# Optimization experiments

Measured on AMD Instinct MI355X. Metric: run time of the kernel, lower is better.

## Reference

```python
import jax, jax.numpy as jnp
import numpy as np

B, K = 512, 64
EBD, VFD = 256, 512
SENS = EBD + VFD            # 768 sensory inputs to layer 0
LAYERS = [512, 256, 64]     # inter, command, motor neurons (NCP wiring)


def _make_layer_params(key, in_features, hidden):
    ks = jax.random.split(key, 9)
    cat = in_features + hidden
    s = 1.0 / np.sqrt(cat)
    def lin(k):
        return jax.random.normal(k, (hidden, cat), dtype=jnp.float32) * s
    # sparsity mask: random NCP-style sparsity on the input block, dense recurrent block
    in_mask = (jax.random.uniform(ks[8], (hidden, in_features)) < 0.5).astype(jnp.float32)
    rec_mask = jnp.ones((hidden, hidden), dtype=jnp.float32)
    mask = jnp.concatenate([in_mask, rec_mask], axis=1)  # (hidden, in+hidden)
    return dict(
        ff1_w=lin(ks[0]), ff1_b=jnp.zeros((hidden,), jnp.float32),
        ff2_w=lin(ks[1]), ff2_b=jnp.zeros((hidden,), jnp.float32),
        ta_w=lin(ks[2]), ta_b=jnp.zeros((hidden,), jnp.float32),
        tb_w=lin(ks[3]), tb_b=jnp.zeros((hidden,), jnp.float32),
        mask=mask,
    )


def setup_inputs() -> dict:
    key = jax.random.key(0)
    k_base, k_vis, k0, k1, k2 = jax.random.split(key, 5)
    inp = {
        'base_expanded_seq': jax.random.normal(k_base, (B, K, EBD), dtype=jnp.float32),
        'visual_seq': jax.random.normal(k_vis, (B, K, VFD), dtype=jnp.float32),
    }
    in_feats = [SENS, LAYERS[0], LAYERS[1]]
    for li, (k, fin, hid) in enumerate(zip([k0, k1, k2], in_feats, LAYERS)):
        p = _make_layer_params(k, fin, hid)
        for name, v in p.items():
            inp[f'l{li}_{name}'] = v
    return inp


def _cfc_cell(x_in, h, ff1_w, ff1_b, ff2_w, ff2_b, ta_w, ta_b, tb_w, tb_b, mask, ts=1.0):
    # ncps CfCCell, mode='default', no backbone, sparsity mask on ff1/ff2
    x = jnp.concatenate([x_in, h], axis=-1)          # (B, in+hidden)
    ff1 = jnp.tanh(x @ (ff1_w * mask).T + ff1_b)
    ff2 = jnp.tanh(x @ (ff2_w * mask).T + ff2_b)
    t_a = x @ ta_w.T + ta_b
    t_b = x @ tb_w.T + tb_b
    t_interp = jax.nn.sigmoid(t_a * ts + t_b)
    return ff1 * (1.0 - t_interp) + t_interp * ff2


def reference(base_expanded_seq, visual_seq,
              l0_ff1_w, l0_ff1_b, l0_ff2_w, l0_ff2_b, l0_ta_w, l0_ta_b, l0_tb_w, l0_tb_b, l0_mask,
              l1_ff1_w, l1_ff1_b, l1_ff2_w, l1_ff2_b, l1_ta_w, l1_ta_b, l1_tb_w, l1_tb_b, l1_mask,
              l2_ff1_w, l2_ff1_b, l2_ff2_w, l2_ff2_b, l2_ta_w, l2_ta_b, l2_tb_w, l2_tb_b, l2_mask):
    layers = [
        (l0_ff1_w, l0_ff1_b, l0_ff2_w, l0_ff2_b, l0_ta_w, l0_ta_b, l0_tb_w, l0_tb_b, l0_mask),
        (l1_ff1_w, l1_ff1_b, l1_ff2_w, l1_ff2_b, l1_ta_w, l1_ta_b, l1_tb_w, l1_tb_b, l1_mask),
        (l2_ff1_w, l2_ff1_b, l2_ff2_w, l2_ff2_b, l2_ta_w, l2_ta_b, l2_tb_w, l2_tb_b, l2_mask),
    ]
    b = base_expanded_seq.shape[0]
    x_seq = jnp.concatenate([base_expanded_seq, visual_seq], axis=-1)  # (B,K,768)
    x_seq = jnp.swapaxes(x_seq, 0, 1)                                  # (K,B,768)
    h_init = tuple(jnp.zeros((b, h), dtype=x_seq.dtype) for h in LAYERS)

    def step(carry, x_t):
        inp = x_t
        new_hs = []
        for p, h in zip(layers, carry):
            h_new = _cfc_cell(inp, h, *p)
            inp = h_new
            new_hs.append(h_new)
        return tuple(new_hs), None

    final_h, _ = jax.lax.scan(step, h_init, x_seq)
    return final_h[-1]  # (B, motor_neurons) = last timestep motor-layer output
```

## Files before the change

### kernel.cpp

```cpp
#include <hip/hip_runtime.h>
#include <cmath>


typedef __attribute__((ext_vector_type(8))) _Float16 half8;
typedef __attribute__((ext_vector_type(4))) float f32x4;

#define DEVINL __device__ __forceinline__

struct Params {
  const float* base;
  const float* visual;
  const _Float16 *w0, *w1, *w2;
  const float *b0f1,*b0f2,*b0ta,*b0tb;
  const float *b1f1,*b1f2,*b1ta,*b1tb;
  const float *b2f1,*b2f2,*b2ta,*b2tb;
  _Float16 *xh0,*xl0,*xh1,*xl1;
  _Float16 *h0h0,*h0h1,*h0l0,*h0l1;
  _Float16 *h1h0,*h1h1,*h1l0,*h1l1;
  _Float16 *h2h0,*h2h1,*h2l0,*h2l1;
  float* out;
};

DEVINL void gload(half8& d, const _Float16* a) {
  asm volatile("global_load_dwordx4 %0, %1, off" : "=v"(d) : "v"(a));
}
template <int V>
DEVINL void vmwait() {
  __builtin_amdgcn_s_waitcnt((V & 15) | (7 << 4) | (15 << 8) | ((V >> 4) << 14));
  __builtin_amdgcn_sched_barrier(0);
}

template <int C, int NC, int D, class AF>
DEVINL void pipe_iter(half8 (&buf)[D][6], f32x4 (&acc)[4], const AF& addr) {
  constexpr int issued = (C + D < NC) ? (C + D) : NC;
  vmwait<6 * (issued - C - 1)>();
  {
    half8 b0 = buf[C % D][0], b1 = buf[C % D][1];
    half8 b2 = buf[C % D][2], b3 = buf[C % D][3];
    half8 ah = buf[C % D][4], al = buf[C % D][5];
    acc[0] = __builtin_amdgcn_mfma_f32_16x16x32_f16(ah, b0, acc[0], 0, 0, 0);
    acc[0] = __builtin_amdgcn_mfma_f32_16x16x32_f16(al, b0, acc[0], 0, 0, 0);
    acc[1] = __builtin_amdgcn_mfma_f32_16x16x32_f16(ah, b1, acc[1], 0, 0, 0);
    acc[1] = __builtin_amdgcn_mfma_f32_16x16x32_f16(al, b1, acc[1], 0, 0, 0);
    acc[2] = __builtin_amdgcn_mfma_f32_16x16x32_f16(ah, b2, acc[2], 0, 0, 0);
    acc[2] = __builtin_amdgcn_mfma_f32_16x16x32_f16(al, b2, acc[2], 0, 0, 0);
    acc[3] = __builtin_amdgcn_mfma_f32_16x16x32_f16(ah, b3, acc[3], 0, 0, 0);
    acc[3] = __builtin_amdgcn_mfma_f32_16x16x32_f16(al, b3, acc[3], 0, 0, 0);
  }
  if constexpr (C + D < NC) {
#pragma unroll
    for (int j = 0; j < 6; ++j) gload(buf[C % D][j], addr(C + D, j));
  }
  if constexpr (C + 1 < NC) pipe_iter<C + 1, NC, D>(buf, acc, addr);
}

template <int NC, class AF>
DEVINL void gemm_pipe(f32x4 (&acc)[4], const AF& addr) {
  constexpr int D = (NC < 4) ? NC : 4;
  half8 buf[D][6];
#pragma unroll
  for (int c = 0; c < D; ++c)
#pragma unroll
    for (int j = 0; j < 6; ++j) gload(buf[c][j], addr(c, j));
  pipe_iter<0, NC, D>(buf, acc, addr);
}

DEVINL void run_xprep(const Params& p, int t, int b ) {
  _Float16* xh = (t & 1) ? p.xh1 : p.xh0;
  _Float16* xl = (t & 1) ? p.xl1 : p.xl0;
  int tid = b * 256 + threadIdx.x;
#pragma unroll
  for (int i = tid; i < 49152; i += 12288) {
    int m = i / 96;
    int k = (i - m * 96) * 8;
    const float* src = (k < 256) ? (p.base + (m * 64 + t) * 256 + k)
                                 : (p.visual + (m * 64 + t) * 512 + (k - 256));
    const f32x4* q = (const f32x4*)src;
    f32x4 v0 = q[0], v1 = q[1];
    half8 hh, ll;
#pragma unroll
    for (int j = 0; j < 4; ++j) {
      _Float16 a = (_Float16)v0[j]; hh[j] = a;     ll[j]     = (_Float16)(v0[j] - (float)a);
      _Float16 c = (_Float16)v1[j]; hh[j + 4] = c; ll[j + 4] = (_Float16)(v1[j] - (float)c);
    }
    int off = (((m >> 4) * 24 + (k >> 5)) * 64 + ((k >> 3) & 3) * 16 + (m & 15)) * 8;
    *(half8*)(xh + off) = hh;
    *(half8*)(xl + off) = ll;
  }
}

template <int L>
DEVINL void run_rec(const Params& p, int t, int b) {
  constexpr int HH = (L == 0) ? 512 : ((L == 1) ? 256 : 64);
  constexpr int NC = (L == 0) ? 40 : ((L == 1) ? 24 : 10);
  constexpr int NCH = HH / 32;

  const int lane = threadIdx.x & 63, wv = threadIdx.x >> 6;
  const int lr = lane & 15, lq = lane >> 4;
  int mt, nt;
  if constexpr (L == 0)      { mt = b >> 5; nt = b & 31; }
  else if constexpr (L == 1) { mt = b >> 4; nt = b & 15; }
  else                       { mt = b >> 2; nt = b & 3; }
  const int m_base = mt * 64 + wv * 16, n0 = nt * 16;
  const int mt16 = mt * 4 + wv;
  const int wbuf = t & 1;

  const _Float16 *hph, *hpl, *pah = nullptr, *pal = nullptr;
  _Float16 *oh, *ol;
  const float *bf1p, *bf2p, *btap, *btbp;
  const _Float16* wpk;
  if constexpr (L == 0) {
    wpk = p.w0 + (nt * 40) * 512 + lane * 8;
    pah = wbuf ? p.xh1 : p.xh0;    pal = wbuf ? p.xl1 : p.xl0;
    hph = wbuf ? p.h0h0 : p.h0h1;  hpl = wbuf ? p.h0l0 : p.h0l1;
    oh  = wbuf ? p.h0h1 : p.h0h0;  ol  = wbuf ? p.h0l1 : p.h0l0;
    bf1p = p.b0f1; bf2p = p.b0f2; btap = p.b0ta; btbp = p.b0tb;
  } else if constexpr (L == 1) {
    wpk = p.w1 + (nt * 24) * 512 + lane * 8;
    pah = wbuf ? p.h0h1 : p.h0h0;  pal = wbuf ? p.h0l1 : p.h0l0;
    hph = wbuf ? p.h1h0 : p.h1h1;  hpl = wbuf ? p.h1l0 : p.h1l1;
    oh  = wbuf ? p.h1h1 : p.h1h0;  ol  = wbuf ? p.h1l1 : p.h1l0;
    bf1p = p.b1f1; bf2p = p.b1f2; btap = p.b1ta; btbp = p.b1tb;
  } else {
    wpk = p.w2 + (nt * 10) * 512 + lane * 8;
    pah = wbuf ? p.h1h1 : p.h1h0;  pal = wbuf ? p.h1l1 : p.h1l0;
    hph = wbuf ? p.h2h0 : p.h2h1;  hpl = wbuf ? p.h2l0 : p.h2l1;
    oh  = wbuf ? p.h2h1 : p.h2h0;  ol  = wbuf ? p.h2l1 : p.h2l0;
    bf1p = p.b2f1; bf2p = p.b2f2; btap = p.b2ta; btbp = p.b2tb;
  }

  f32x4 acc[4];
#pragma unroll
  for (int g = 0; g < 4; ++g) acc[g] = f32x4{0.f, 0.f, 0.f, 0.f};

  const int lane8 = lane * 8;
  auto addr = [&](int c, int j) -> const _Float16* {
    if constexpr (L == 0) {
      if (j < 4) return wpk + (j * (32 * 40) + c) * 512;
      if (c < 24) return ((j == 4) ? pah : pal) + (mt16 * 24 + c) * 512 + lane8;
      return ((j == 4) ? hph : hpl) + (mt16 * 16 + (c - 24)) * 512 + lane8;
    } else if constexpr (L == 1) {
      if (j < 4) return wpk + (j * (16 * 24) + c) * 512;
      if (c < 16) return ((j == 4) ? pah : pal) + (mt16 * 16 + c) * 512 + lane8;
      return ((j == 4) ? hph : hpl) + (mt16 * 8 + (c - 16)) * 512 + lane8;
    } else {
      if (j < 4) return wpk + (j * (4 * 10) + c) * 512;
      if (c < 8) return ((j == 4) ? pah : pal) + (mt16 * 8 + c) * 512 + lane8;
      return ((j == 4) ? hph : hpl) + (mt16 * 2 + (c - 8)) * 512 + lane8;
    }
  };
  gemm_pipe<NC>(acc, addr);

  const int n = n0 + lr;
  const float bff1 = bf1p[n], bff2 = bf2p[n], bta = btap[n], btb = btbp[n];
  const int obase = ((m_base >> 4) * NCH + (n >> 5)) * 512 + ((n >> 3) & 3) * 128 + (n & 7);
#pragma unroll
  for (int r = 0; r < 4; ++r) {
    const int row = m_base + lq * 4 + r;
    const int lrr = lq * 4 + r;
    float a0 = acc[0][r], a1 = acc[1][r], a2 = acc[2][r], a3 = acc[3][r];
    float vf1 = a0 + bff1;
    float vf2 = a1 + bff2;
    float vt  = (a2 + bta) + (a3 + btb);
    float ff1 = tanhf(vf1);
    float ff2 = tanhf(vf2);
    float ti  = 1.0f / (1.0f + __expf(-vt));
    float hv  = ff1 + ti * (ff2 - ff1);
    _Float16 hh = (_Float16)hv;
    oh[obase + lrr * 8] = hh;
    ol[obase + lrr * 8] = (_Float16)(hv - (float)hh);
    if constexpr (L == 2) {
      if (t == 63) p.out[row * 64 + n] = hv;
    }
  }
}

__global__ __launch_bounds__(256, 2) void cfc_step(Params p, int s) {
  const int bid = blockIdx.x;
  if (bid < 48)       { int t = s + 1; if (t >= 0 && t < 64) run_xprep(p, t, bid); }
  else if (bid < 304) { int t = s;     if (t >= 0 && t < 64) run_rec<0>(p, t, bid - 48); }
  else if (bid < 432) { int t = s - 1; if (t >= 0 && t < 64) run_rec<1>(p, t, bid - 304); }
  else                { int t = s - 2; if (t >= 0 && t < 64) run_rec<2>(p, t, bid - 432); }
}

__global__ void prep_w_pk(const float* __restrict__ w, const float* __restrict__ mask,
                          _Float16* __restrict__ dst, int WK, int total) {
  int i = blockIdx.x * 256 + threadIdx.x;
  if (i >= total) return;
  int e = i & 7, lane = (i >> 3) & 63, rem = i >> 9;
  int NCk = WK >> 5;
  int c = rem % NCk, nt = rem / NCk;
  int n = nt * 16 + (lane & 15);
  int k = c * 32 + (lane >> 4) * 8 + e;
  float v = w[n * WK + k];
  if (mask) v *= mask[n * WK + k];
  dst[i] = (_Float16)v;
}

__global__ void zero_kernel(unsigned* __restrict__ p, int n) {
  int i = blockIdx.x * 256 + threadIdx.x;
  if (i < n) p[i] = 0u;
}

extern "C" void kernel_launch(void* const* d_in, const int* in_sizes, int n_in,
                              void* d_out, int out_size, void* d_ws, size_t ws_size,
                              hipStream_t stream) {
  _Float16* w0  = (_Float16*)d_ws;
  _Float16* w1  = w0 + 2621440;
  _Float16* w2  = w1 + 786432;
  _Float16* xh0 = w2 + 81920;
  _Float16* xl0 = xh0 + 393216;
  _Float16* xh1 = xl0 + 393216;
  _Float16* xl1 = xh1 + 393216;
  _Float16* hb  = xl1 + 393216;
  _Float16* h0h0 = hb;            _Float16* h0h1 = h0h0 + 262144;
  _Float16* h0l0 = h0h1 + 262144; _Float16* h0l1 = h0l0 + 262144;
  _Float16* h1h0 = h0l1 + 262144; _Float16* h1h1 = h1h0 + 131072;
  _Float16* h1l0 = h1h1 + 131072; _Float16* h1l1 = h1l0 + 131072;
  _Float16* h2h0 = h1l1 + 131072; _Float16* h2h1 = h2h0 + 32768;
  _Float16* h2l0 = h2h1 + 32768;  _Float16* h2l1 = h2l0 + 32768;

  const int h_uints = 1703936 / 2;
  zero_kernel<<<(h_uints + 255) / 256, 256, 0, stream>>>((unsigned*)hb, h_uints);

  const float* F = nullptr;
  auto in = [&](int i) { return (const float*)d_in[i]; };

  prep_w_pk<<<2560, 256, 0, stream>>>(in(2),  in(10), w0 + 0 * 655360, 1280, 655360);
  prep_w_pk<<<2560, 256, 0, stream>>>(in(4),  in(10), w0 + 1 * 655360, 1280, 655360);
  prep_w_pk<<<2560, 256, 0, stream>>>(in(6),  F,      w0 + 2 * 655360, 1280, 655360);
  prep_w_pk<<<2560, 256, 0, stream>>>(in(8),  F,      w0 + 3 * 655360, 1280, 655360);
  prep_w_pk<<<768,  256, 0, stream>>>(in(11), in(19), w1 + 0 * 196608, 768,  196608);
  prep_w_pk<<<768,  256, 0, stream>>>(in(13), in(19), w1 + 1 * 196608, 768,  196608);
  prep_w_pk<<<768,  256, 0, stream>>>(in(15), F,      w1 + 2 * 196608, 768,  196608);
  prep_w_pk<<<768,  256, 0, stream>>>(in(17), F,      w1 + 3 * 196608, 768,  196608);
  prep_w_pk<<<80,   256, 0, stream>>>(in(20), in(28), w2 + 0 * 20480,  320,  20480);
  prep_w_pk<<<80,   256, 0, stream>>>(in(22), in(28), w2 + 1 * 20480,  320,  20480);
  prep_w_pk<<<80,   256, 0, stream>>>(in(24), F,      w2 + 2 * 20480,  320,  20480);
  prep_w_pk<<<80,   256, 0, stream>>>(in(26), F,      w2 + 3 * 20480,  320,  20480);

  Params p;
  p.base = in(0); p.visual = in(1);
  p.w0 = w0; p.w1 = w1; p.w2 = w2;
  p.b0f1 = in(3);  p.b0f2 = in(5);  p.b0ta = in(7);  p.b0tb = in(9);
  p.b1f1 = in(12); p.b1f2 = in(14); p.b1ta = in(16); p.b1tb = in(18);
  p.b2f1 = in(21); p.b2f2 = in(23); p.b2ta = in(25); p.b2tb = in(27);
  p.xh0 = xh0; p.xl0 = xl0; p.xh1 = xh1; p.xl1 = xl1;
  p.h0h0 = h0h0; p.h0h1 = h0h1; p.h0l0 = h0l0; p.h0l1 = h0l1;
  p.h1h0 = h1h0; p.h1h1 = h1h1; p.h1l0 = h1l0; p.h1l1 = h1l1;
  p.h2h0 = h2h0; p.h2h1 = h2h1; p.h2l0 = h2l0; p.h2l1 = h2l1;
  p.out = (float*)d_out;

  for (int s = -1; s < 66; ++s) {
    cfc_step<<<464, 256, 0, stream>>>(p, s);
  }
}
```

Before: 1.162 ms.

## Replace per-step kernel launches with persistent kernel and global atomic barrier

Replaces the 67 back-to-back launches of the step kernel with a single persistent kernel that loops over steps and synchronises all 464 blocks through an atomic counter barrier with release/acquire fences. The aim is to remove per-launch overhead and the gaps between kernels. A host occupancy check falls back to the old multi-launch path if not all blocks can be co-resident. The spin barrier adds contention and assumes co-residency holds at run time; if it does not, the kernel could deadlock.

```diff
diff --git a/kernel.cpp b/kernel.cpp
--- a/kernel.cpp
+++ b/kernel.cpp
@@ -175,12 +175,35 @@
   }
 }
 
-__global__ __launch_bounds__(256, 2) void cfc_step(Params p, int s) {
-  const int bid = blockIdx.x;
+DEVINL void run_roles(const Params& p, int s, int bid) {
   if (bid < 48)       { int t = s + 1; if (t >= 0 && t < 64) run_xprep(p, t, bid); }
   else if (bid < 304) { int t = s;     if (t >= 0 && t < 64) run_rec<0>(p, t, bid - 48); }
   else if (bid < 432) { int t = s - 1; if (t >= 0 && t < 64) run_rec<1>(p, t, bid - 304); }
   else                { int t = s - 2; if (t >= 0 && t < 64) run_rec<2>(p, t, bid - 432); }
+}
+
+__global__ __launch_bounds__(256, 2) void cfc_persist(Params p, unsigned* ctr) {
+  const int bid = blockIdx.x;
+  unsigned target = 0;
+  for (int s = -1; s < 66; ++s) {
+    run_roles(p, s, bid);
+    if (s < 65) {
+      target += 464;
+      __syncthreads();
+      __builtin_amdgcn_fence(__ATOMIC_RELEASE, "agent");
+      if (threadIdx.x == 0) {
+        __hip_atomic_fetch_add(ctr, 1u, __ATOMIC_RELAXED, __HIP_MEMORY_SCOPE_AGENT);
+        while (__hip_atomic_load(ctr, __ATOMIC_RELAXED, __HIP_MEMORY_SCOPE_AGENT) < target)
+          __builtin_amdgcn_s_sleep(2);
+      }
+      __syncthreads();
+      __builtin_amdgcn_fence(__ATOMIC_ACQUIRE, "agent");
+    }
+  }
+}
+
+__global__ __launch_bounds__(256, 2) void cfc_step(Params p, int s) {
+  run_roles(p, s, blockIdx.x);
 }
 
 __global__ void prep_w_pk(const float* __restrict__ w, const float* __restrict__ mask,
@@ -219,8 +242,9 @@
   _Float16* h1l0 = h1h1 + 131072; _Float16* h1l1 = h1l0 + 131072;
   _Float16* h2h0 = h1l1 + 131072; _Float16* h2h1 = h2h0 + 32768;
   _Float16* h2l0 = h2h1 + 32768;  _Float16* h2l1 = h2l0 + 32768;
-
-  const int h_uints = 1703936 / 2;
+  unsigned* ctr = (unsigned*)(h2l1 + 32768);
+
+  const int h_uints = 1703936 / 2 + 64;
   zero_kernel<<<(h_uints + 255) / 256, 256, 0, stream>>>((unsigned*)hb, h_uints);
 
   const float* F = nullptr;
@@ -251,7 +275,25 @@
   p.h2h0 = h2h0; p.h2h1 = h2h1; p.h2l0 = h2l0; p.h2l1 = h2l1;
   p.out = (float*)d_out;
 
-  for (int s = -1; s < 66; ++s) {
-    cfc_step<<<464, 256, 0, stream>>>(p, s);
-  }
-}
+  static int persist_ok = -1;
+  if (persist_ok < 0) {
+    int maxb = 0;
+    hipError_t e1 = hipOccupancyMaxActiveBlocksPerMultiprocessor(
+        &maxb, (const void*)cfc_persist, 256, 0);
+    int ncu = 0;
+    hipDeviceProp_t prop;
+    int dev = 0;
+    if (hipGetDevice(&dev) == hipSuccess &&
+        hipGetDeviceProperties(&prop, dev) == hipSuccess)
+      ncu = prop.multiProcessorCount;
+    persist_ok = (e1 == hipSuccess && maxb * ncu >= 464) ? 1 : 0;
+  }
+
+  if (persist_ok == 1) {
+    cfc_persist<<<464, 256, 0, stream>>>(p, ctr);
+  } else {
+    for (int s = -1; s < 66; ++s) {
+      cfc_step<<<464, 256, 0, stream>>>(p, s);
+    }
+  }
+}
```

After: 1.167 ms. Within noise of the previous version (+0.4%).
